# Optimization experiments

Hardware: AMD Instinct MI355X
Metric: run time of the kernel (lower is better)

Reference implementation:

```python
import jax, jax.numpy as jnp
import numpy as np

G = 64        # graphs per batch
NPG = 1024    # nodes per graph (static)
DEG = 8       # avg degree
INF = 128
HID = 256
OUT = 256
N = G * NPG
E = N * DEG
K1 = 512      # ceil(0.5 * 1024)
K2 = 256      # ceil(0.5 * 512)
EPS = 1e-5


def setup_inputs() -> dict:
    key = jax.random.key(0)
    ks = jax.random.split(key, 12)
    s = 0.05
    x = jax.random.normal(ks[0], (N, INF), jnp.float32)
    off = (jnp.arange(G, dtype=jnp.int32) * NPG)[:, None]
    src = (jax.random.randint(ks[1], (G, NPG * DEG), 0, NPG, jnp.int32) + off).reshape(-1)
    dst = (jax.random.randint(ks[2], (G, NPG * DEG), 0, NPG, jnp.int32) + off).reshape(-1)
    return {
        'x': x, 'src': src, 'dst': dst,
        'W_rel1': jax.random.normal(ks[3], (INF, HID), jnp.float32) * s,
        'b_rel1': jnp.zeros((HID,), jnp.float32),
        'W_root1': jax.random.normal(ks[4], (INF, HID), jnp.float32) * s,
        'g1': jnp.ones((HID,), jnp.float32), 'bt1': jnp.zeros((HID,), jnp.float32),
        'p1': jax.random.normal(ks[5], (HID,), jnp.float32) * s,
        'g2': jnp.ones((HID,), jnp.float32), 'bt2': jnp.zeros((HID,), jnp.float32),
        'W_rel2': jax.random.normal(ks[6], (HID, HID), jnp.float32) * s,
        'b_rel2': jnp.zeros((HID,), jnp.float32),
        'W_root2': jax.random.normal(ks[7], (HID, HID), jnp.float32) * s,
        'p2': jax.random.normal(ks[8], (HID,), jnp.float32) * s,
        'Wl': jax.random.normal(ks[9], (2 * HID, OUT), jnp.float32) * s,
        'bl': jnp.zeros((OUT,), jnp.float32),
    }


def _bn(x, g, b):
    # training-mode BatchNorm over nodes (biased variance), as nn.BatchNorm1d
    m = x.mean(0)
    v = x.var(0)
    return (x - m) * jax.lax.rsqrt(v + EPS) * g + b


def _conv(x, src, dst, emask, W_rel, b_rel, W_root):
    # GraphConv: sum_{j->i} x_j, then lin_rel(aggr) + lin_root(x)
    msg = x[src]                                    # [E, F] gather
    if emask is not None:
        msg = jnp.where(emask[:, None], msg, 0.0)   # dropped edges contribute 0
    agg = jax.ops.segment_sum(msg, dst, num_segments=x.shape[0])
    return agg @ W_rel + b_rel + x @ W_root


def _pool(x, src, dst, emask, p, n, k):
    # TopKPooling: score = tanh((x.p)/||p||); keep top-k per graph; x *= score
    score = jnp.tanh((x @ p) / jnp.linalg.norm(p))  # [G*n]
    vals, idx = jax.lax.top_k(score.reshape(G, n), k)   # [G, k] per-graph
    perm = (idx + (jnp.arange(G, dtype=jnp.int32) * n)[:, None]).reshape(-1)
    xn = x[perm] * vals.reshape(-1)[:, None]        # [G*k, F]
    # remap old node ids -> new ids; -1 marks dropped nodes
    mapping = jnp.full((G * n,), -1, jnp.int32).at[perm].set(
        jnp.arange(G * k, dtype=jnp.int32))
    ns, nd = mapping[src], mapping[dst]
    nmask = emask & (ns >= 0) & (nd >= 0)
    ns = jnp.where(nmask, ns, 0)
    nd = jnp.where(nmask, nd, 0)
    return xn, ns, nd, nmask


def reference(x, src, dst, W_rel1, b_rel1, W_root1, g1, bt1, p1,
              g2, bt2, W_rel2, b_rel2, W_root2, p2, Wl, bl):
    act = lambda v: jax.nn.gelu(v, approximate=False)
    h = _conv(x, src, dst, None, W_rel1, b_rel1, W_root1)
    h = _bn(act(h), g1, bt1)
    h, s1, d1, m1 = _pool(h, src, dst, jnp.ones((E,), bool), p1, NPG, K1)
    hg = h.reshape(G, K1, HID)
    x1 = jnp.concatenate([hg.max(1), hg.mean(1)], axis=1)   # [G, 2H] gmp|gap
    h = act(_bn(h, g2, bt2))
    h = _conv(h, s1, d1, m1, W_rel2, b_rel2, W_root2)
    h, s2, d2, m2 = _pool(h, s1, d1, m1, p2, K1, K2)
    hg = h.reshape(G, K2, HID)
    x2 = jnp.concatenate([hg.max(1), hg.mean(1)], axis=1)
    return (x1 + x2) @ Wl + bl                              # [G, OUT]
```

## Files before the change

### kernel.cpp

```cpp
#include <hip/hip_runtime.h>
#include <hip/hip_bf16.h>
#include <float.h>

#define GG    64
#define NPG   1024
#define EPG   8192
#define NE    524288
#define FIN   128
#define HID   256
#define K1    512
#define K2    256
#define NN0   65536
#define NN1   32768
#define NN2   16384
#define EPSBN 1e-5f

typedef _Float16 f16x8 __attribute__((ext_vector_type(8)));
typedef _Float16 f16x4 __attribute__((ext_vector_type(4)));
typedef float f32x4 __attribute__((ext_vector_type(4)));

__device__ __forceinline__ float gelu_exact(float v) {
    return 0.5f * v * (1.0f + erff(v * 0.7071067811865476f));
}

__device__ __forceinline__ void gld16(const void* g, void* lds) {
    __builtin_amdgcn_global_load_lds(
        (const __attribute__((address_space(1))) unsigned int*)g,
        (__attribute__((address_space(3))) unsigned int*)lds, 16, 0, 0);
}

__global__ __launch_bounds__(512) void k_prepcsr(
        const int* __restrict__ src, const int* __restrict__ dst,
        int* __restrict__ rowp, int* __restrict__ ssrc, int* __restrict__ map1,
        const float* __restrict__ Wrel1, const float* __restrict__ Wroot1,
        const float* __restrict__ Wrel2, const float* __restrict__ Wroot2,
        const float* __restrict__ p2,
        _Float16* __restrict__ W1h, _Float16* __restrict__ W2h,
        float* __restrict__ q2, float* __restrict__ stats1,
        float* __restrict__ stats2) {
    __shared__ int cnt[NPG];
    __shared__ int sa[NPG];
    __shared__ int sb[NPG];
    __shared__ float red[256];
    const int b = blockIdx.x, tid = threadIdx.x;
    if (b < 64) {
        const int g = b;
        const int eb = g * EPG;
        for (int i = g * 512 + tid; i < NN0; i += GG * 512) map1[i] = -1;
        for (int i = tid; i < NPG; i += 512) cnt[i] = 0;
        __syncthreads();
        for (int e = tid; e < EPG; e += 512)
            atomicAdd(&cnt[dst[eb + e] & (NPG - 1)], 1);
        __syncthreads();
        for (int i = tid; i < NPG; i += 512) sa[i] = cnt[i];
        __syncthreads();
        int* cur = sa; int* nxt = sb;
        for (int d = 1; d < NPG; d <<= 1) {
            for (int i = tid; i < NPG; i += 512)
                nxt[i] = cur[i] + ((i >= d) ? cur[i - d] : 0);
            __syncthreads();
            int* t = cur; cur = nxt; nxt = t;
        }
        for (int i = tid; i < NPG; i += 512) {
            const int st = cur[i] - cnt[i];
            rowp[g * (NPG + 1) + i] = st;
            cnt[i] = st;
        }
        if (tid == 0) rowp[g * (NPG + 1) + NPG] = EPG;
        __syncthreads();
        for (int e = tid; e < EPG; e += 512) {
            const int d = dst[eb + e] & (NPG - 1);
            const int p = atomicAdd(&cnt[d], 1);
            ssrc[eb + p] = src[eb + e] & (NPG - 1);
        }
    } else if (b < 192) {
        const int i = (b - 64) * 512 + tid;
        const int n = i >> 8, k = i & 255;
        const float v = (k < FIN) ? Wrel1[k * HID + n] : Wroot1[(k - FIN) * HID + n];
        W1h[((k >> 3) << 11) + (n << 3) + (k & 7)] = (_Float16)v;
    } else if (b < 448) {
        const int i = (b - 192) * 512 + tid;
        const int n = i >> 9, k = i & 511;
        const float v = (k < HID) ? Wrel2[k * HID + n] : Wroot2[(k - HID) * HID + n];
        W2h[((k >> 3) << 11) + (n << 3) + (k & 7)] = (_Float16)v;
    } else if (b == 448) {
        if (tid < 256) { const float pv = p2[tid]; red[tid] = pv * pv; }
        __syncthreads();
        for (int s = 128; s > 0; s >>= 1) {
            if (tid < s) red[tid] += red[tid + s];
            __syncthreads();
        }
        if (tid < 256) q2[tid] = p2[tid] * rsqrtf(red[0]);
    } else {
        stats1[tid] = 0.f;
        stats2[tid] = 0.f;
    }
}

__global__ __launch_bounds__(256) void k_agg1(const float* __restrict__ x,
        const int* __restrict__ rowp, const int* __restrict__ ssrc,
        _Float16* __restrict__ A1) {
    const int b = blockIdx.x;
    const int g = b & 63;
    const int ng = b >> 6;
    const int tid = threadIdx.x;
    const int ln = tid & 31;
    const int node = (ng << 3) + (tid >> 5);
    const int s0 = rowp[g * (NPG + 1) + node];
    const int s1 = rowp[g * (NPG + 1) + node + 1];
    const float4* x4 = reinterpret_cast<const float4*>(x);
    const size_t gb = (size_t)(g << 10) * 32;
    const int* sp = ssrc + (size_t)g * EPG;
    float4 acc = make_float4(0.f, 0.f, 0.f, 0.f);
    for (int j = s0; j < s1; ++j) {
        const float4 v = x4[gb + (size_t)sp[j] * 32 + ln];
        acc.x += v.x; acc.y += v.y; acc.z += v.z; acc.w += v.w;
    }
    const size_t rb = ((size_t)((g << 10) + node)) * 256;
    *reinterpret_cast<f16x4*>(&A1[rb + (ln << 2)]) =
        (f16x4){(_Float16)acc.x, (_Float16)acc.y, (_Float16)acc.z, (_Float16)acc.w};
    const float4 xv = x4[gb + (size_t)node * 32 + ln];
    *reinterpret_cast<f16x4*>(&A1[rb + 128 + (ln << 2)]) =
        (f16x4){(_Float16)xv.x, (_Float16)xv.y, (_Float16)xv.z, (_Float16)xv.w};
}

__global__ __launch_bounds__(256) void k_agg2(const _Float16* __restrict__ A2r,
        const int* __restrict__ rowp, const int* __restrict__ ssrc,
        const int* __restrict__ perm1, const int* __restrict__ map1,
        _Float16* __restrict__ A2w) {
    const int b = blockIdx.x;
    const int g = b & 63;
    const int ng = b >> 6;
    const int tid = threadIdx.x;
    const int ln = tid & 63;
    const int ni = (ng << 2) + (tid >> 6);
    const int on = perm1[(g << 9) + ni] & (NPG - 1);
    const int s0 = rowp[g * (NPG + 1) + on];
    const int s1 = rowp[g * (NPG + 1) + on + 1];
    const int* sp = ssrc + (size_t)g * EPG;
    const int* mp = map1 + ((size_t)g << 10);
    float4 acc = make_float4(0.f, 0.f, 0.f, 0.f);
    for (int j = s0; j < s1; ++j) {
        const int ms = mp[sp[j]];
        if (ms < 0) continue;
        const f16x4 v = *reinterpret_cast<const f16x4*>(
            &A2r[(size_t)ms * 512 + 256 + (ln << 2)]);
        acc.x += (float)v[0]; acc.y += (float)v[1];
        acc.z += (float)v[2]; acc.w += (float)v[3];
    }
    *reinterpret_cast<f16x4*>(&A2w[((size_t)((g << 9) + ni)) * 512 + (ln << 2)]) =
        (f16x4){(_Float16)acc.x, (_Float16)acc.y, (_Float16)acc.z, (_Float16)acc.w};
}

template<int K, int EPI, int MCH>
__global__ __launch_bounds__(512, 2) void k_gemmB(
        const _Float16* __restrict__ A, const _Float16* __restrict__ B,
        const float* __restrict__ bias, _Float16* __restrict__ C,
        float* __restrict__ stats, const float* __restrict__ qv2,
        float* __restrict__ scores, int M) {
    __shared__ _Float16 Bs[256 * 256];
    __shared__ float csum[256];
    __shared__ float csq[256];
    const int tid = threadIdx.x;
    const int l = tid & 63, w = tid >> 6;
    constexpr int BM = 8 * MCH * 16;
    const int m0 = blockIdx.x * BM;
    const int r16 = l & 15, kg = l >> 4;

    f32x4 acc[MCH][16] = {};
    constexpr int PH = K / 256;

#pragma unroll
    for (int ph = 0; ph < PH; ++ph) {
        if (ph) __syncthreads();
        for (int u = tid; u < 8192; u += 512)
            gld16(B + ((size_t)ph * 8192 + u) * 8, (char*)Bs + u * 16);
        asm volatile("s_waitcnt vmcnt(0)" ::: "memory");
        __syncthreads();

#pragma unroll
        for (int ks = 0; ks < 8; ++ks) {
            f16x8 a[MCH];
#pragma unroll
            for (int mc = 0; mc < MCH; ++mc) {
                const int mrow = m0 + (w * MCH + mc) * 16 + r16;
                a[mc] = *reinterpret_cast<const f16x8*>(
                    A + (size_t)mrow * K + ph * 256 + ks * 32 + kg * 8);
            }
#pragma unroll
            for (int ni = 0; ni < 16; ++ni) {
                const int brow = ni * 16 + r16;
                const int c = ks * 4 + kg;
                const f16x8 bf = *reinterpret_cast<const f16x8*>(
                    (const char*)Bs + ((c << 8) + brow) * 16);
#pragma unroll
                for (int mc = 0; mc < MCH; ++mc)
                    acc[mc][ni] = __builtin_amdgcn_mfma_f32_16x16x32_f16(
                        a[mc], bf, acc[mc][ni], 0, 0, 0);
            }
        }
    }

    if (EPI == 1) {
        __syncthreads();
        if (tid < 256) { csum[tid] = 0.f; csq[tid] = 0.f; }
        __syncthreads();
    }

    float sp[MCH][4];
    if (EPI == 2) {
#pragma unroll
        for (int mc = 0; mc < MCH; ++mc)
#pragma unroll
            for (int r = 0; r < 4; ++r) sp[mc][r] = 0.f;
    }
#pragma unroll
    for (int ni = 0; ni < 16; ++ni) {
        const int col = ni * 16 + r16;
        const float bc = bias[col];
        const float qvn = (EPI == 2) ? qv2[col] : 0.f;
        float sA = 0.f, qA = 0.f;
#pragma unroll
        for (int mc = 0; mc < MCH; ++mc) {
#pragma unroll
            for (int r = 0; r < 4; ++r) {
                const int row = m0 + (w * MCH + mc) * 16 + (kg << 2) + r;
                float t = acc[mc][ni][r] + bc;
                if (EPI == 1) {
                    t = gelu_exact(t);
                    sA += t;
                    qA += t * t;
                }
                if (EPI == 2) sp[mc][r] += t * qvn;
                C[(size_t)row * 256 + col] = (_Float16)t;
            }
        }
        if (EPI == 1) {
            unsafeAtomicAdd(&csum[col], sA);
            unsafeAtomicAdd(&csq[col], qA);
        }
    }
    if (EPI == 1) {
        __syncthreads();
        if (tid < 256) {
            unsafeAtomicAdd(&stats[tid], csum[tid]);
            unsafeAtomicAdd(&stats[HID + tid], csq[tid]);
        }
    }
    if (EPI == 2) {
#pragma unroll
        for (int mc = 0; mc < MCH; ++mc)
#pragma unroll
            for (int r = 0; r < 4; ++r) {
                float s = sp[mc][r];
                s += __shfl_xor(s, 1);
                s += __shfl_xor(s, 2);
                s += __shfl_xor(s, 4);
                s += __shfl_xor(s, 8);
                if (r16 == 0)
                    scores[m0 + (w * MCH + mc) * 16 + (kg << 2) + r] = s;
            }
    }
}

__global__ __launch_bounds__(256) void k_finalize1(const float* __restrict__ stats,
        const float* __restrict__ g1, const float* __restrict__ bt1,
        const float* __restrict__ p1, float* __restrict__ scale,
        float* __restrict__ shift, float* __restrict__ q, float* __restrict__ r) {
    __shared__ float red[256];
    const int c = threadIdx.x;
    const float m = stats[c] * (1.f / NN0);
    const float v = stats[HID + c] * (1.f / NN0) - m * m;
    const float sc = g1[c] * rsqrtf(v + EPSBN);
    const float sh = bt1[c] - m * sc;
    scale[c] = sc;
    shift[c] = sh;
    const float pv = p1[c];
    red[c] = pv * pv;
    __syncthreads();
    for (int s = 128; s > 0; s >>= 1) {
        if (c < s) red[c] += red[c + s];
        __syncthreads();
    }
    const float inv = rsqrtf(red[0]);
    q[c] = sc * pv * inv;
    __syncthreads();
    red[c] = sh * pv * inv;
    __syncthreads();
    for (int s = 128; s > 0; s >>= 1) {
        if (c < s) red[c] += red[c + s];
        __syncthreads();
    }
    if (c == 0) r[0] = red[0];
}

__global__ __launch_bounds__(256) void k_finalize2(const float* __restrict__ stats,
        const float* __restrict__ g2, const float* __restrict__ bt2,
        float* __restrict__ scale, float* __restrict__ shift) {
    const int c = threadIdx.x;
    const float m = stats[c] * (1.f / NN1);
    const float v = stats[HID + c] * (1.f / NN1) - m * m;
    const float sc = g2[c] * rsqrtf(v + EPSBN);
    scale[c] = sc;
    shift[c] = bt2[c] - m * sc;
}

__global__ __launch_bounds__(256) void k_score(const _Float16* __restrict__ H,
        const float* __restrict__ q, const float* __restrict__ r,
        float* __restrict__ out) {
    const int node = blockIdx.x * 4 + (threadIdx.x >> 6);
    const int lane = threadIdx.x & 63;
    const f16x4 h = *reinterpret_cast<const f16x4*>(H + (size_t)node * HID + (lane << 2));
    const float4 qv = *reinterpret_cast<const float4*>(q + (lane << 2));
    float d = (float)h[0] * qv.x + (float)h[1] * qv.y +
              (float)h[2] * qv.z + (float)h[3] * qv.w;
#pragma unroll
    for (int off = 32; off > 0; off >>= 1) d += __shfl_xor(d, off);
    if (lane == 0) out[node] = d + (r ? r[0] : 0.f);
}

template<int NN_, int KK_, int NT_>
__global__ __launch_bounds__(NT_) void k_topk(const float* __restrict__ scores,
        int nparts, int pstride, int* __restrict__ perm,
        float* __restrict__ vals, int* __restrict__ mapping) {
    __shared__ float s[NN_];
    __shared__ int id[NN_];
    const int g = blockIdx.x, tid = threadIdx.x;
    for (int i = tid; i < NN_; i += NT_) {
        float raw = 0.f;
        for (int p = 0; p < nparts; ++p)
            raw += scores[(size_t)p * pstride + g * NN_ + i];
        s[i] = tanhf(raw);
        id[i] = i;
    }
    __syncthreads();
    for (int k = 2; k <= NN_; k <<= 1) {
        for (int j = k >> 1; j > 0; j >>= 1) {
            for (int t = tid; t < NN_; t += NT_) {
                const int ixj = t ^ j;
                if (ixj > t) {
                    const bool desc = ((t & k) == 0);
                    const float s1 = s[t], s2 = s[ixj];
                    const int i1 = id[t], i2 = id[ixj];
                    const bool inOrder = (s1 > s2) || (s1 == s2 && i1 < i2);
                    if (inOrder != desc) { s[t] = s2; s[ixj] = s1; id[t] = i2; id[ixj] = i1; }
                }
            }
            __syncthreads();
        }
    }
    for (int i = tid; i < KK_; i += NT_) {
        const int oid = id[i];
        perm[g * KK_ + i] = g * NN_ + oid;
        vals[g * KK_ + i] = s[i];
        if (mapping) mapping[g * NN_ + oid] = g * KK_ + i;
    }
}

__global__ __launch_bounds__(256) void k_pool1p(const _Float16* __restrict__ HG,
        const int* __restrict__ perm, const float* __restrict__ vals,
        const float* __restrict__ scale1, const float* __restrict__ shift1,
        float* __restrict__ pmax, float* __restrict__ psum,
        float* __restrict__ psq) {
    const int b = blockIdx.x;
    const int g = b >> 3, ig = b & 7;
    const int c = threadIdx.x;
    const float sc = scale1[c], sh = shift1[c];
    float mx = -FLT_MAX, sm = 0.f, sq = 0.f;
    for (int i = ig * 64; i < ig * 64 + 64; ++i) {
        const int idx = (g << 9) + i;
        const int srow = perm[idx];
        const float val = vals[idx];
        const float hv = (float)HG[(size_t)srow * HID + c];
        const float xn = (hv * sc + sh) * val;
        mx = fmaxf(mx, xn);
        sm += xn;
        sq += xn * xn;
    }
    pmax[b * 256 + c] = mx;
    psum[b * 256 + c] = sm;
    psq[b * 256 + c] = sq;
}

__global__ __launch_bounds__(256) void k_pool1r(const float* __restrict__ pmax,
        const float* __restrict__ psum, const float* __restrict__ psq,
        float* __restrict__ X1, float* __restrict__ stats2) {
    const int g = blockIdx.x, c = threadIdx.x;
    float mx = -FLT_MAX, sm = 0.f, sq = 0.f;
    for (int ig = 0; ig < 8; ++ig) {
        const int o = ((g << 3) + ig) * 256 + c;
        mx = fmaxf(mx, pmax[o]);
        sm += psum[o];
        sq += psq[o];
    }
    X1[g * 512 + c] = mx;
    X1[g * 512 + 256 + c] = sm * (1.f / K1);
    unsafeAtomicAdd(&stats2[c], sm);
    unsafeAtomicAdd(&stats2[HID + c], sq);
}

__global__ __launch_bounds__(256) void k_h2in(const _Float16* __restrict__ HG,
        const int* __restrict__ perm, const float* __restrict__ vals,
        const float* __restrict__ scale1, const float* __restrict__ shift1,
        const float* __restrict__ scale2, const float* __restrict__ shift2,
        _Float16* __restrict__ A2) {
    const int i = blockIdx.x * 256 + threadIdx.x;
    const int idx = i >> 6, c4 = i & 63;
    const int srow = perm[idx];
    const float val = vals[idx];
    const f16x4 h = *reinterpret_cast<const f16x4*>(&HG[(size_t)srow * HID + (c4 << 2)]);
    const float4 s1 = reinterpret_cast<const float4*>(scale1)[c4];
    const float4 b1 = reinterpret_cast<const float4*>(shift1)[c4];
    const float4 s2 = reinterpret_cast<const float4*>(scale2)[c4];
    const float4 b2 = reinterpret_cast<const float4*>(shift2)[c4];
    const float x0 = ((float)h[0] * s1.x + b1.x) * val;
    const float x1 = ((float)h[1] * s1.y + b1.y) * val;
    const float x2 = ((float)h[2] * s1.z + b1.z) * val;
    const float x3 = ((float)h[3] * s1.w + b1.w) * val;
    *reinterpret_cast<f16x4*>(&A2[(size_t)idx * 512 + 256 + (c4 << 2)]) =
        (f16x4){(_Float16)gelu_exact(x0 * s2.x + b2.x),
                (_Float16)gelu_exact(x1 * s2.y + b2.y),
                (_Float16)gelu_exact(x2 * s2.z + b2.z),
                (_Float16)gelu_exact(x3 * s2.w + b2.w)};
}

__global__ __launch_bounds__(256) void k_x2p(const _Float16* __restrict__ H2,
        const int* __restrict__ perm, const float* __restrict__ vals,
        float* __restrict__ pmax, float* __restrict__ psum) {
    const int b = blockIdx.x;
    const int g = b >> 3, ig = b & 7;
    const int c = threadIdx.x;
    float mx = -FLT_MAX, sm = 0.f;
    for (int i = ig * 32; i < ig * 32 + 32; ++i) {
        const int idx = (g << 8) + i;
        const int srow = perm[idx];
        const float v = (float)H2[(size_t)srow * HID + c] * vals[idx];
        mx = fmaxf(mx, v);
        sm += v;
    }
    pmax[b * 256 + c] = mx;
    psum[b * 256 + c] = sm;
}

__global__ __launch_bounds__(256) void k_x2final(const float* __restrict__ pmax,
        const float* __restrict__ psum, const float* __restrict__ X1,
        const float* __restrict__ Wl, const float* __restrict__ bl,
        float* __restrict__ out) {
    __shared__ float sx2[512];
    const int g = blockIdx.x, c = threadIdx.x;
    float mx = -FLT_MAX, sm = 0.f;
    for (int ig = 0; ig < 8; ++ig) {
        const int o = ((g << 3) + ig) * 256 + c;
        mx = fmaxf(mx, pmax[o]);
        sm += psum[o];
    }
    sx2[c] = mx;
    sx2[256 + c] = sm * (1.f / K2);
    __syncthreads();
    float acc = bl[c];
    for (int k = 0; k < 512; ++k) {
        const float xv = X1[g * 512 + k] + sx2[k];
        acc = fmaf(xv, Wl[k * HID + c], acc);
    }
    out[g * HID + c] = acc;
}

extern "C" void kernel_launch(void* const* d_in, const int* in_sizes, int n_in,
                              void* d_out, int out_size, void* d_ws, size_t ws_size,
                              hipStream_t stream) {
    (void)in_sizes; (void)n_in; (void)out_size; (void)ws_size;
    const float* x       = (const float*)d_in[0];
    const int*   src     = (const int*)  d_in[1];
    const int*   dst     = (const int*)  d_in[2];
    const float* W_rel1  = (const float*)d_in[3];
    const float* b_rel1  = (const float*)d_in[4];
    const float* W_root1 = (const float*)d_in[5];
    const float* g1      = (const float*)d_in[6];
    const float* bt1     = (const float*)d_in[7];
    const float* p1      = (const float*)d_in[8];
    const float* g2      = (const float*)d_in[9];
    const float* bt2     = (const float*)d_in[10];
    const float* W_rel2  = (const float*)d_in[11];
    const float* b_rel2  = (const float*)d_in[12];
    const float* W_root2 = (const float*)d_in[13];
    const float* p2      = (const float*)d_in[14];
    const float* Wl      = (const float*)d_in[15];
    const float* bl      = (const float*)d_in[16];
    float* out = (float*)d_out;

    char* w = (char*)d_ws;
    size_t off = 0;
    auto alloc = [&](size_t bytes) -> void* {
        void* p = w + off;
        off += (bytes + 255) & ~(size_t)255;
        return p;
    };
    _Float16* A1  = (_Float16*)alloc((size_t)NN0 * 256 * 2);
    _Float16* HG  = (_Float16*)alloc((size_t)NN0 * 256 * 2);
    _Float16* H2  = (_Float16*)alloc((size_t)NN1 * 256 * 2);
    int*   ROWP   = (int*)  alloc((size_t)GG * (NPG + 1) * 4);
    int*   SSRC   = (int*)  alloc((size_t)NE * 4);
    float* SCORES = (float*)alloc((size_t)NN0 * 4);
    int*   PERM1  = (int*)  alloc((size_t)NN1 * 4);
    float* VALS1  = (float*)alloc((size_t)NN1 * 4);
    int*   MAP1   = (int*)  alloc((size_t)NN0 * 4);
    int*   PERM2  = (int*)  alloc((size_t)NN2 * 4);
    float* VALS2  = (float*)alloc((size_t)NN2 * 4);
    float* STATS1 = (float*)alloc(512 * 4);
    float* STATS2 = (float*)alloc(512 * 4);
    float* SCALE1 = (float*)alloc(256 * 4);
    float* SHIFT1 = (float*)alloc(256 * 4);
    float* Q1     = (float*)alloc(256 * 4);
    float* R1     = (float*)alloc(256);
    float* SCALE2 = (float*)alloc(256 * 4);
    float* SHIFT2 = (float*)alloc(256 * 4);
    float* Q2     = (float*)alloc(256 * 4);
    _Float16* W1h = (_Float16*)alloc((size_t)256 * 256 * 2);
    _Float16* W2h = (_Float16*)alloc((size_t)256 * 512 * 2);
    float* X1     = (float*)alloc((size_t)GG * 512 * 4);
    float* PMAX   = (float*)alloc((size_t)512 * 256 * 4);
    float* PSUM   = (float*)alloc((size_t)512 * 256 * 4);
    float* PSQ    = (float*)alloc((size_t)512 * 256 * 4);
    _Float16* A2 = A1;

    k_prepcsr<<<450, 512, 0, stream>>>(src, dst, ROWP, SSRC, MAP1,
        W_rel1, W_root1, W_rel2, W_root2, p2, W1h, W2h, Q2, STATS1, STATS2);
    k_agg1<<<8192, 256, 0, stream>>>(x, ROWP, SSRC, A1);
    k_gemmB<256, 1, 2><<<256, 512, 0, stream>>>(A1, W1h, b_rel1, HG, STATS1,
        nullptr, nullptr, NN0);
    k_finalize1<<<1, 256, 0, stream>>>(STATS1, g1, bt1, p1, SCALE1, SHIFT1, Q1, R1);
    k_score<<<NN0 / 4, 256, 0, stream>>>(HG, Q1, R1, SCORES);
    k_topk<NPG, K1, 512><<<GG, 512, 0, stream>>>(SCORES, 1, 0, PERM1, VALS1, MAP1);
    k_pool1p<<<512, 256, 0, stream>>>(HG, PERM1, VALS1, SCALE1, SHIFT1, PMAX, PSUM, PSQ);
    k_pool1r<<<GG, 256, 0, stream>>>(PMAX, PSUM, PSQ, X1, STATS2);
    k_finalize2<<<1, 256, 0, stream>>>(STATS2, g2, bt2, SCALE2, SHIFT2);
    k_h2in<<<8192, 256, 0, stream>>>(HG, PERM1, VALS1, SCALE1, SHIFT1,
        SCALE2, SHIFT2, A2);
    k_agg2<<<8192, 256, 0, stream>>>(A2, ROWP, SSRC, PERM1, MAP1, A2);
    k_gemmB<512, 2, 1><<<256, 512, 0, stream>>>(A2, W2h, b_rel2, H2, nullptr,
        Q2, SCORES, NN1);
    k_topk<K1, K2, 256><<<GG, 256, 0, stream>>>(SCORES, 1, 0, PERM2, VALS2, nullptr);
    k_x2p<<<512, 256, 0, stream>>>(H2, PERM2, VALS2, PMAX, PSUM);
    k_x2final<<<GG, 256, 0, stream>>>(PMAX, PSUM, X1, Wl, bl, out);
}
```

Baseline: 252.5 us.

## Run GEMM blocks with 1024 threads and split output columns across waves

The fused GEMM kernel now launches 1024-thread blocks, 16 waves each. Every wave handles one 16-row strip and a slice of the output columns (NSPLIT column groups), where before each wave held several row chunks and all 16 column tiles. This is meant to spread the shared-LDS weight load and the MFMA work over more waves to hide latency, with fewer accumulators per thread. In return each wave reloads A fragments and issues fewer MFMAs per load. For the second GEMM the score dot-product becomes partial per column half, so top-k is changed to sum two score slices.

```diff
diff --git a/kernel.cpp b/kernel.cpp
--- a/kernel.cpp
+++ b/kernel.cpp
@@ -152,8 +152,8 @@
         (f16x4){(_Float16)acc.x, (_Float16)acc.y, (_Float16)acc.z, (_Float16)acc.w};
 }
 
-template<int K, int EPI, int MCH>
-__global__ __launch_bounds__(512, 2) void k_gemmB(
+template<int K, int EPI, int NSPLIT>
+__global__ __launch_bounds__(1024, 4) void k_gemmB(
         const _Float16* __restrict__ A, const _Float16* __restrict__ B,
         const float* __restrict__ bias, _Float16* __restrict__ C,
         float* __restrict__ stats, const float* __restrict__ qv2,
@@ -163,40 +163,36 @@
     __shared__ float csq[256];
     const int tid = threadIdx.x;
     const int l = tid & 63, w = tid >> 6;
-    constexpr int BM = 8 * MCH * 16;
+    const int rc = w / NSPLIT, ch = w % NSPLIT;
+    constexpr int NIW = 16 / NSPLIT;
+    constexpr int BM = (16 / NSPLIT) * 16;
     const int m0 = blockIdx.x * BM;
     const int r16 = l & 15, kg = l >> 4;
-
-    f32x4 acc[MCH][16] = {};
+    const int mrow = m0 + rc * 16 + r16;
+
+    f32x4 acc[NIW] = {};
     constexpr int PH = K / 256;
 
 #pragma unroll
     for (int ph = 0; ph < PH; ++ph) {
         if (ph) __syncthreads();
-        for (int u = tid; u < 8192; u += 512)
+        for (int u = tid; u < 8192; u += 1024)
             gld16(B + ((size_t)ph * 8192 + u) * 8, (char*)Bs + u * 16);
         asm volatile("s_waitcnt vmcnt(0)" ::: "memory");
         __syncthreads();
 
 #pragma unroll
         for (int ks = 0; ks < 8; ++ks) {
-            f16x8 a[MCH];
-#pragma unroll
-            for (int mc = 0; mc < MCH; ++mc) {
-                const int mrow = m0 + (w * MCH + mc) * 16 + r16;
-                a[mc] = *reinterpret_cast<const f16x8*>(
-                    A + (size_t)mrow * K + ph * 256 + ks * 32 + kg * 8);
-            }
-#pragma unroll
-            for (int ni = 0; ni < 16; ++ni) {
-                const int brow = ni * 16 + r16;
+            const f16x8 a = *reinterpret_cast<const f16x8*>(
+                A + (size_t)mrow * K + ph * 256 + ks * 32 + kg * 8);
+#pragma unroll
+            for (int ni = 0; ni < NIW; ++ni) {
+                const int brow = (ch * NIW + ni) * 16 + r16;
                 const int c = ks * 4 + kg;
                 const f16x8 bf = *reinterpret_cast<const f16x8*>(
                     (const char*)Bs + ((c << 8) + brow) * 16);
-#pragma unroll
-                for (int mc = 0; mc < MCH; ++mc)
-                    acc[mc][ni] = __builtin_amdgcn_mfma_f32_16x16x32_f16(
-                        a[mc], bf, acc[mc][ni], 0, 0, 0);
+                acc[ni] = __builtin_amdgcn_mfma_f32_16x16x32_f16(
+                    a, bf, acc[ni], 0, 0, 0);
             }
         }
     }
@@ -207,33 +203,28 @@
         __syncthreads();
     }
 
-    float sp[MCH][4];
+    float sp[4];
     if (EPI == 2) {
 #pragma unroll
-        for (int mc = 0; mc < MCH; ++mc)
-#pragma unroll
-            for (int r = 0; r < 4; ++r) sp[mc][r] = 0.f;
-    }
-#pragma unroll
-    for (int ni = 0; ni < 16; ++ni) {
-        const int col = ni * 16 + r16;
+        for (int r = 0; r < 4; ++r) sp[r] = 0.f;
+    }
+#pragma unroll
+    for (int ni = 0; ni < NIW; ++ni) {
+        const int col = (ch * NIW + ni) * 16 + r16;
         const float bc = bias[col];
         const float qvn = (EPI == 2) ? qv2[col] : 0.f;
         float sA = 0.f, qA = 0.f;
 #pragma unroll
-        for (int mc = 0; mc < MCH; ++mc) {
-#pragma unroll
-            for (int r = 0; r < 4; ++r) {
-                const int row = m0 + (w * MCH + mc) * 16 + (kg << 2) + r;
-                float t = acc[mc][ni][r] + bc;
-                if (EPI == 1) {
-                    t = gelu_exact(t);
-                    sA += t;
-                    qA += t * t;
-                }
-                if (EPI == 2) sp[mc][r] += t * qvn;
-                C[(size_t)row * 256 + col] = (_Float16)t;
+        for (int r = 0; r < 4; ++r) {
+            const int row = m0 + rc * 16 + (kg << 2) + r;
+            float t = acc[ni][r] + bc;
+            if (EPI == 1) {
+                t = gelu_exact(t);
+                sA += t;
+                qA += t * t;
             }
+            if (EPI == 2) sp[r] += t * qvn;
+            C[(size_t)row * 256 + col] = (_Float16)t;
         }
         if (EPI == 1) {
             unsafeAtomicAdd(&csum[col], sA);
@@ -249,17 +240,15 @@
     }
     if (EPI == 2) {
 #pragma unroll
-        for (int mc = 0; mc < MCH; ++mc)
-#pragma unroll
-            for (int r = 0; r < 4; ++r) {
-                float s = sp[mc][r];
-                s += __shfl_xor(s, 1);
-                s += __shfl_xor(s, 2);
-                s += __shfl_xor(s, 4);
-                s += __shfl_xor(s, 8);
-                if (r16 == 0)
-                    scores[m0 + (w * MCH + mc) * 16 + (kg << 2) + r] = s;
-            }
+        for (int r = 0; r < 4; ++r) {
+            float s = sp[r];
+            s += __shfl_xor(s, 1);
+            s += __shfl_xor(s, 2);
+            s += __shfl_xor(s, 4);
+            s += __shfl_xor(s, 8);
+            if (r16 == 0)
+                scores[(size_t)ch * M + m0 + rc * 16 + (kg << 2) + r] = s;
+        }
     }
 }
 
@@ -526,7 +515,7 @@
     k_prepcsr<<<450, 512, 0, stream>>>(src, dst, ROWP, SSRC, MAP1,
         W_rel1, W_root1, W_rel2, W_root2, p2, W1h, W2h, Q2, STATS1, STATS2);
     k_agg1<<<8192, 256, 0, stream>>>(x, ROWP, SSRC, A1);
-    k_gemmB<256, 1, 2><<<256, 512, 0, stream>>>(A1, W1h, b_rel1, HG, STATS1,
+    k_gemmB<256, 1, 1><<<256, 1024, 0, stream>>>(A1, W1h, b_rel1, HG, STATS1,
         nullptr, nullptr, NN0);
     k_finalize1<<<1, 256, 0, stream>>>(STATS1, g1, bt1, p1, SCALE1, SHIFT1, Q1, R1);
     k_score<<<NN0 / 4, 256, 0, stream>>>(HG, Q1, R1, SCORES);
@@ -537,9 +526,9 @@
     k_h2in<<<8192, 256, 0, stream>>>(HG, PERM1, VALS1, SCALE1, SHIFT1,
         SCALE2, SHIFT2, A2);
     k_agg2<<<8192, 256, 0, stream>>>(A2, ROWP, SSRC, PERM1, MAP1, A2);
-    k_gemmB<512, 2, 1><<<256, 512, 0, stream>>>(A2, W2h, b_rel2, H2, nullptr,
+    k_gemmB<512, 2, 2><<<256, 1024, 0, stream>>>(A2, W2h, b_rel2, H2, nullptr,
         Q2, SCORES, NN1);
-    k_topk<K1, K2, 256><<<GG, 256, 0, stream>>>(SCORES, 1, 0, PERM2, VALS2, nullptr);
+    k_topk<K1, K2, 256><<<GG, 256, 0, stream>>>(SCORES, 2, NN1, PERM2, VALS2, nullptr);
     k_x2p<<<512, 256, 0, stream>>>(H2, PERM2, VALS2, PMAX, PSUM);
     k_x2final<<<GG, 256, 0, stream>>>(PMAX, PSUM, X1, Wl, bl, out);
 }
```

Result: slower. 271.8 us (+7.6%).
